# Kernel optimization log

Measured on AMD Instinct MI355X. Metric: run time of the kernel, lower is better.

## Reference

```python
import jax, jax.numpy as jnp
import numpy as np

N = 8192      # grid points along the differentiated axis (axis=0)
B = 4096      # trailing batch/feature dim
S = 7         # stencil width (order=2, acc=4)


def _make_offsets(n, s):
    # Interior stencil is centered (-3..3); near boundaries the stencil is
    # shifted one-sided so that i + off stays in [0, n-1], matching the
    # precomputed one-sided boundary stencils of a non-uniform FD operator.
    i = np.arange(n)[:, None]                      # [n, 1]
    base = np.arange(s)[None, :] - s // 2          # [1, s]
    idx = np.clip(i + base, 0, n - 1)
    # de-duplicate clipped indices by re-spreading near boundaries
    lo_shift = np.maximum(0, (s // 2) - np.arange(n))[:, None]
    hi_shift = np.maximum(0, (s // 2) - (n - 1 - np.arange(n)))[:, None]
    idx = i + base + lo_shift - hi_shift           # valid, distinct indices
    return (idx - i).astype(np.int32)              # offsets relative to i


def setup_inputs() -> dict:
    key = jax.random.key(0)
    k1, k2 = jax.random.split(key)
    y = jax.random.normal(k1, (N, B), dtype=jnp.float32)
    all_coefficients = jax.random.normal(k2, (N, S), dtype=jnp.float32)
    all_offsets = jnp.asarray(_make_offsets(N, S))  # int32 [N, S]
    return {"y": y, "all_coefficients": all_coefficients, "all_offsets": all_offsets}


def reference(y, all_coefficients, all_offsets):
    # axis = 0, so y is already in 'moved' layout y_m.
    # Original: for each i, yd[i] = sum_s ws[i,s] * y[i + offs[i,s]]
    # (sequential fori_loop). Vectorized over all grid points i:
    n = y.shape[0]
    idxs = jnp.arange(n, dtype=all_offsets.dtype)[:, None] + all_offsets  # [n, S]
    stencil = jnp.take(y, idxs, axis=0)              # [n, S, B] gather
    yd = jnp.einsum('ns,ns...->n...', all_coefficients, stencil)
    return yd
```

## Files before the change

kernel.cpp:

```cpp
#include <hip/hip_runtime.h>
#include <hip/hip_bf16.h>


#define FD_N 8192
#define FD_B 4096
#define FD_S 7
#define FD_R 8
#define HALO 3
#define WIN  (FD_R + 2 * HALO)

__global__ __launch_bounds__(256, 1) void
_FinDiffNonUniform_51608327029442_kernel(const float* __restrict__ y,
                                         const float* __restrict__ coef,
                                         const int*   __restrict__ offs,
                                         float*       __restrict__ out) {
    const int strip = blockIdx.x >> 2;
    const int n0    = strip * FD_R;
    const int b     = ((blockIdx.x & 3) << 10) + (threadIdx.x << 2);

    if (strip > 0 && strip < (FD_N / FD_R - 1)) {
        const float* ybase = y + (size_t)(n0 - HALO) * FD_B + b;

        float4 w[WIN];
#pragma unroll
        for (int j = 0; j < WIN; ++j)
            w[j] = *reinterpret_cast<const float4*>(ybase + (size_t)j * FD_B);

        float c[FD_R][FD_S];
#pragma unroll
        for (int r = 0; r < FD_R; ++r)
#pragma unroll
            for (int s = 0; s < FD_S; ++s)
                c[r][s] = coef[(size_t)(n0 + r) * FD_S + s];

        float4 acc[FD_R];
#pragma unroll
        for (int r = 0; r < FD_R; ++r)
            acc[r] = make_float4(0.f, 0.f, 0.f, 0.f);

#pragma unroll
        for (int j = 0; j < WIN; ++j) {
#pragma unroll
            for (int r = 0; r < FD_R; ++r) {
                const int s = j - r;
                if (s >= 0 && s < FD_S) {
                    const float cc = c[r][s];
                    acc[r].x += cc * w[j].x;
                    acc[r].y += cc * w[j].y;
                    acc[r].z += cc * w[j].z;
                    acc[r].w += cc * w[j].w;
                }
            }
        }

#pragma unroll
        for (int r = 0; r < FD_R; ++r)
            *reinterpret_cast<float4*>(out + (size_t)(n0 + r) * FD_B + b) = acc[r];
    } else {
#pragma unroll
        for (int r = 0; r < FD_R; ++r) {
            const int n = n0 + r;
            float4 acc = make_float4(0.f, 0.f, 0.f, 0.f);
#pragma unroll
            for (int s = 0; s < FD_S; ++s) {
                const float cc = coef[n * FD_S + s];
                const int   o  = offs[n * FD_S + s];
                const float4 v =
                    *reinterpret_cast<const float4*>(y + (size_t)(n + o) * FD_B + b);
                acc.x += cc * v.x;
                acc.y += cc * v.y;
                acc.z += cc * v.z;
                acc.w += cc * v.w;
            }
            *reinterpret_cast<float4*>(out + (size_t)n * FD_B + b) = acc;
        }
    }
}

extern "C" void kernel_launch(void* const* d_in, const int* in_sizes, int n_in,
                              void* d_out, int out_size, void* d_ws, size_t ws_size,
                              hipStream_t stream) {
    const float* y    = (const float*)d_in[0];
    const float* coef = (const float*)d_in[1];
    const int*   offs = (const int*)d_in[2];
    float*       out  = (float*)d_out;

    const int blocks = (FD_N / FD_R) * (FD_B / 1024);
    _FinDiffNonUniform_51608327029442_kernel<<<blocks, 256, 0, stream>>>(y, coef, offs, out);
}
```

Measured before the change: 237.1 us.

## Shrink row strips, remap blocks across XCDs, use nontemporal stores

Cuts rows per block from 8 to 2, raising block count and occupancy but lowering halo reuse (8 loads per 2 outputs instead of 14 per 8). Block IDs are remapped so consecutive strips of a column chunk land on the same XCD, keeping overlapping halo rows in that XCD's L2. Output stores become nontemporal to avoid polluting cache, and launch_bounds no longer caps residency at one block. The extra halo reads raise L2 traffic, which the XCD-local mapping is meant to absorb.

New measurement: 232.3 us. -2.0%, faster.

```diff
diff --git a/kernel.cpp b/kernel.cpp
--- a/kernel.cpp
+++ b/kernel.cpp
@@ -1,31 +1,32 @@
 #include <hip/hip_runtime.h>
-#include <hip/hip_bf16.h>
 
 
-#define FD_N 8192
-#define FD_B 4096
-#define FD_S 7
-#define FD_R 8
-#define HALO 3
-#define WIN  (FD_R + 2 * HALO)
+#define FD_N   8192
+#define FD_B   4096
+#define FD_S   7
+#define FD_R   2
+#define HALO   3
+#define WIN    (FD_R + 2 * HALO)
+#define NSTRIP (FD_N / FD_R)
+#define NCHUNK 4
+#define NWG    (NSTRIP * NCHUNK)
+#define NXCD   8
 
-__global__ __launch_bounds__(256, 1) void
+typedef float v4f __attribute__((ext_vector_type(4)));
+
+__global__ __launch_bounds__(256) void
 _FinDiffNonUniform_51608327029442_kernel(const float* __restrict__ y,
                                          const float* __restrict__ coef,
                                          const int*   __restrict__ offs,
                                          float*       __restrict__ out) {
-    const int strip = blockIdx.x >> 2;
+    const int bid   = blockIdx.x;
+    const int id    = (bid & (NXCD - 1)) * (NWG / NXCD) + (bid >> 3);
+    const int strip = id & (NSTRIP - 1);
+    const int chunk = id >> 12;
     const int n0    = strip * FD_R;
-    const int b     = ((blockIdx.x & 3) << 10) + (threadIdx.x << 2);
+    const int b     = (chunk << 10) + (threadIdx.x << 2);
 
-    if (strip > 0 && strip < (FD_N / FD_R - 1)) {
-        const float* ybase = y + (size_t)(n0 - HALO) * FD_B + b;
-
-        float4 w[WIN];
-#pragma unroll
-        for (int j = 0; j < WIN; ++j)
-            w[j] = *reinterpret_cast<const float4*>(ybase + (size_t)j * FD_B);
-
+    if (strip >= 2 && strip <= NSTRIP - 3) {
         float c[FD_R][FD_S];
 #pragma unroll
         for (int r = 0; r < FD_R; ++r)
@@ -33,46 +34,49 @@
             for (int s = 0; s < FD_S; ++s)
                 c[r][s] = coef[(size_t)(n0 + r) * FD_S + s];
 
-        float4 acc[FD_R];
+        const float* ybase = y + (size_t)(n0 - HALO) * FD_B + b;
+
+        v4f w[WIN];
+#pragma unroll
+        for (int j = 0; j < WIN; ++j)
+            w[j] = *reinterpret_cast<const v4f*>(ybase + (size_t)j * FD_B);
+
+        asm volatile("" ::: "memory");
+
+        v4f acc[FD_R];
 #pragma unroll
         for (int r = 0; r < FD_R; ++r)
-            acc[r] = make_float4(0.f, 0.f, 0.f, 0.f);
+            acc[r] = (v4f){0.f, 0.f, 0.f, 0.f};
 
 #pragma unroll
         for (int j = 0; j < WIN; ++j) {
 #pragma unroll
             for (int r = 0; r < FD_R; ++r) {
                 const int s = j - r;
-                if (s >= 0 && s < FD_S) {
-                    const float cc = c[r][s];
-                    acc[r].x += cc * w[j].x;
-                    acc[r].y += cc * w[j].y;
-                    acc[r].z += cc * w[j].z;
-                    acc[r].w += cc * w[j].w;
-                }
+                if (s >= 0 && s < FD_S)
+                    acc[r] += c[r][s] * w[j];
             }
         }
 
 #pragma unroll
         for (int r = 0; r < FD_R; ++r)
-            *reinterpret_cast<float4*>(out + (size_t)(n0 + r) * FD_B + b) = acc[r];
+            __builtin_nontemporal_store(
+                acc[r], reinterpret_cast<v4f*>(out + (size_t)(n0 + r) * FD_B + b));
     } else {
 #pragma unroll
         for (int r = 0; r < FD_R; ++r) {
             const int n = n0 + r;
-            float4 acc = make_float4(0.f, 0.f, 0.f, 0.f);
+            v4f acc = (v4f){0.f, 0.f, 0.f, 0.f};
 #pragma unroll
             for (int s = 0; s < FD_S; ++s) {
-                const float cc = coef[n * FD_S + s];
-                const int   o  = offs[n * FD_S + s];
-                const float4 v =
-                    *reinterpret_cast<const float4*>(y + (size_t)(n + o) * FD_B + b);
-                acc.x += cc * v.x;
-                acc.y += cc * v.y;
-                acc.z += cc * v.z;
-                acc.w += cc * v.w;
+                const float cc = coef[(size_t)n * FD_S + s];
+                const int   o  = offs[(size_t)n * FD_S + s];
+                const v4f   v  =
+                    *reinterpret_cast<const v4f*>(y + (size_t)(n + o) * FD_B + b);
+                acc += cc * v;
             }
-            *reinterpret_cast<float4*>(out + (size_t)n * FD_B + b) = acc;
+            __builtin_nontemporal_store(
+                acc, reinterpret_cast<v4f*>(out + (size_t)n * FD_B + b));
         }
     }
 }
@@ -85,6 +89,5 @@
     const int*   offs = (const int*)d_in[2];
     float*       out  = (float*)d_out;
 
-    const int blocks = (FD_N / FD_R) * (FD_B / 1024);
-    _FinDiffNonUniform_51608327029442_kernel<<<blocks, 256, 0, stream>>>(y, coef, offs, out);
+    _FinDiffNonUniform_51608327029442_kernel<<<NWG, 256, 0, stream>>>(y, coef, offs, out);
 }
```
